# Performance work log

Hardware: AMD Instinct MI355X
Metric: run time of the kernel (lower is better)

## Reference

```python
import jax, jax.numpy as jnp
import numpy as np

SR = 16000
NFFT = 512
HOP = 160
D_MIC = 0.05
SPEED = 343.0
PRE = 0.97
ALPHA, BETA, GAMMA = 0.5, 0.3, 0.2
MAXLEN = 40000
N_ANGLES = 181
T = 6400000

# ---- constant buffers (match torch register_buffer setup) ----
_freqs = np.fft.rfftfreq(NFFT, 1.0 / SR).astype(np.float32)            # [F]
_angles = np.linspace(0.0, 180.0, N_ANGLES).astype(np.float32)         # [A]
_tau = -(D_MIC * np.cos(np.deg2rad(_angles))) / SPEED
_phase = (2.0 * np.pi) * _tau[:, None] * _freqs[None, :]               # [A, F]
STEER_R = jnp.asarray(np.cos(_phase).astype(np.float32))
STEER_I = jnp.asarray(np.sin(_phase).astype(np.float32))
ANGLE_GRID = jnp.asarray(_angles)

_wl = SPEED / (_freqs + 1e-6)
_sr_res = D_MIC / _wl
_spatial = 1.0 / (1.0 + np.exp(-4.0 * (_sr_res - 0.1)))
_fw = 1.0 - np.exp(-((_freqs - SR / 6.0) ** 2) / (2.0 * (SR / 4.0) ** 2))
_alias = np.where(_sr_res < 0.5, np.ones_like(_freqs), np.exp(-2.0 * (_sr_res - 0.5) ** 2))
_cw = (_spatial * _fw * _alias)[None, :]
FREQ_W = jnp.asarray((_cw / (_cw.sum() + 1e-6)).astype(np.float32))    # [1, F]

_w = np.exp(np.linspace(-2.0, 0.0, MAXLEN).astype(np.float32))
TEMPORAL = jnp.asarray((_w / _w.sum()).reshape(1, 1, -1))              # [1,1,MAXLEN]

_n = np.arange(NFFT)
WINDOW = jnp.asarray((0.5 - 0.5 * np.cos(2.0 * np.pi * _n / NFFT)).astype(np.float32))
N_FRAMES = (T - NFFT) // HOP + 1
FRAME_IDX = jnp.asarray((np.arange(N_FRAMES)[:, None] * HOP + _n[None, :]).astype(np.int32))


def _stft(x):
    # x: [1, 1, T] -> (real, imag) each [1, F, n_frames]
    frames = x[:, 0, :][:, FRAME_IDX] * WINDOW       # [1, n_frames, NFFT]
    spec = jnp.fft.rfft(frames, axis=-1)             # [1, n_frames, F]
    spec = jnp.swapaxes(spec, 1, 2)                  # [1, F, n_frames]
    return jnp.real(spec).astype(jnp.float32), jnp.imag(spec).astype(jnp.float32)


def _preproc(w):
    w = w * (1.0 / 32768.0)
    w = w - jnp.mean(w, axis=-1, keepdims=True)
    return jnp.concatenate([w[:, :, :1], w[:, :, 1:] - PRE * w[:, :, :-1]], axis=-1)


def _mvdr_scores(mic_wav_0, mic_wav_1):
    r0, i0 = _stft(_preproc(mic_wav_0))
    r1, i1 = _stft(_preproc(mic_wav_1))
    p0 = r0 * r0 + i0 * i0
    p1 = r1 * r1 + i1 * i1
    r01 = r0 * r1 + i0 * i1
    i01 = i0 * r1 - r0 * i1
    wts = TEMPORAL[..., : p0.shape[-1]]
    R00 = (p0 * wts).sum(2)                          # [1, F]
    R11 = (p1 * wts).sum(2)
    R01r = (r01 * wts).sum(2)
    R01i = (i01 * wts).sum(2)
    trace = (R00 + R11) * 0.5
    det = R00 * R11 - (R01r ** 2 + R01i ** 2) + 1e-6 * trace
    inv_det = 1.0 / det
    iR00 = R11 * inv_det
    iR11 = R00 * inv_det
    iR01r = -R01r * inv_det
    iR01i = -R01i * inv_det
    qf = iR01r * STEER_R + iR01i * STEER_I           # [A, F] (B=1 broadcast)
    qf = iR00 + iR11 + qf + qf
    mvdr = 1.0 / (qf + 1e-6)
    logp = jnp.log(mvdr + 1e-6)
    geometric = jnp.exp((logp * FREQ_W).sum(-1))     # [A]
    arithmetic = (mvdr * FREQ_W).sum(-1)
    peak_w = jax.nn.softmax(mvdr + mvdr, axis=-1)
    peak = (mvdr * peak_w * FREQ_W).sum(-1)
    return ALPHA * geometric + BETA * arithmetic + GAMMA * peak


def setup_inputs() -> dict:
    key = jax.random.key(0)
    k0, k1 = jax.random.split(key)
    mic_wav_0 = jax.random.normal(k0, (1, 1, T), jnp.float32) * 8000.0
    noise = jax.random.normal(k1, (1, 1, T), jnp.float32) * 8000.0
    # correlated second channel with a small time shift (plausible TDOA)
    mic_wav_1 = 0.7 * jnp.roll(mic_wav_0, 3, axis=-1) + 0.3 * noise
    return {"mic_wav_0": mic_wav_0, "mic_wav_1": mic_wav_1}


def reference(mic_wav_0, mic_wav_1):
    scores = _mvdr_scores(mic_wav_0, mic_wav_1)      # [A]
    return ANGLE_GRID[jnp.argmax(scores, axis=-1)]
```

## Files before the change

### kernel.cpp

```cpp
#include <hip/hip_runtime.h>
#include <math.h>

#ifndef M_PI
#define M_PI 3.14159265358979323846
#endif

#define HOP 160
#define NBLK_MAX 2048
#define PSLOTS 1036

__device__ __forceinline__ float wave_reduce(float v) {
    for (int off = 32; off > 0; off >>= 1) v += __shfl_down(v, off, 64);
    return v;
}

__device__ __forceinline__ void dft8(float* xr, float* xi) {
    const float s = 0.70710678118654752440f;
    float t0r = xr[0] + xr[4], t0i = xi[0] + xi[4];
    float t1r = xr[0] - xr[4], t1i = xi[0] - xi[4];
    float t2r = xr[2] + xr[6], t2i = xi[2] + xi[6];
    float t3r = xr[2] - xr[6], t3i = xi[2] - xi[6];
    float E0r = t0r + t2r, E0i = t0i + t2i;
    float E2r = t0r - t2r, E2i = t0i - t2i;
    float E1r = t1r + t3i, E1i = t1i - t3r;
    float E3r = t1r - t3i, E3i = t1i + t3r;
    float u0r = xr[1] + xr[5], u0i = xi[1] + xi[5];
    float u1r = xr[1] - xr[5], u1i = xi[1] - xi[5];
    float u2r = xr[3] + xr[7], u2i = xi[3] + xi[7];
    float u3r = xr[3] - xr[7], u3i = xi[3] - xi[7];
    float O0r = u0r + u2r, O0i = u0i + u2i;
    float O2r = u0r - u2r, O2i = u0i - u2i;
    float O1r = u1r + u3i, O1i = u1i - u3r;
    float O3r = u1r - u3i, O3i = u1i + u3r;
    float T1r = s * (O1r + O1i), T1i = s * (O1i - O1r);
    float T2r = O2i,             T2i = -O2r;
    float T3r = s * (O3i - O3r), T3i = -s * (O3r + O3i);
    xr[0] = E0r + O0r; xi[0] = E0i + O0i;
    xr[4] = E0r - O0r; xi[4] = E0i - O0i;
    xr[1] = E1r + T1r; xi[1] = E1i + T1i;
    xr[5] = E1r - T1r; xi[5] = E1i - T1i;
    xr[2] = E2r + T2r; xi[2] = E2i + T2i;
    xr[6] = E2r - T2r; xi[6] = E2i - T2i;
    xr[3] = E3r + T3r; xi[3] = E3i + T3i;
    xr[7] = E3r - T3r; xi[7] = E3i - T3i;
}

__device__ __forceinline__ void cmul_t(float& zr, float& zi, float tr, float ti) {
    float r = zr * tr - zi * ti;
    float i = zr * ti + zi * tr;
    zr = r; zi = i;
}

__global__ __launch_bounds__(256) void stft_fft_kernel(
        const float* __restrict__ x0, const float* __restrict__ x1,
        float* __restrict__ partials,
        int T, int nframes, int fpb, int nblocks, int cs,
        float invS, float kslope)
{
    __shared__ float smem[4608];
    const int tid = threadIdx.x;
    const int w = tid >> 6, l = tid & 63;
    float* buf = smem + w * 1152;
    const int n0 = l & 7, hi = l >> 3;
    const int pl = (64 - l) & 63;
    const int b1r = n0 + 72 * hi;
    const int b2w = hi + 72 * n0;

    float c0 = 0.f, c1 = 0.f;
    {
        int lo = blockIdx.x * cs;
        int hi2 = lo + cs; if (hi2 > T) hi2 = T;
        for (int i = lo + tid; i < hi2; i += 256) { c0 += x0[i]; c1 += x1[i]; }
        c0 = wave_reduce(c0); c1 = wave_reduce(c1);
        if (l == 0) { smem[2 * w] = c0; smem[2 * w + 1] = c1; }
    }
    __syncthreads();
    const float c0T = (smem[0] + smem[2]) + (smem[4] + smem[6]);
    const float c1T = (smem[1] + smem[3]) + (smem[5] + smem[7]);
    __syncthreads();

    float winv[8];
#pragma unroll
    for (int j = 0; j < 8; ++j)
        winv[j] = (0.5f - 0.5f * cosf((float)(2.0 * M_PI / 512.0) * (float)(l + 64 * j)))
                  * (1.0f / 32768.0f);
    float t1r[8], t1i[8], t2r[8], t2i[8];
#pragma unroll
    for (int j = 0; j < 8; ++j) {
        sincosf((float)(-2.0 * M_PI / 64.0) * (float)(j * hi), &t1i[j], &t1r[j]);
        sincosf((float)(-2.0 * M_PI / 512.0) * (float)(j * l), &t2i[j], &t2r[j]);
    }

    float A[8];
    float Wr[5], Wi[5];
    float L0r = 0.f, L0i = 0.f, L7r = 0.f, L7i = 0.f;
#pragma unroll
    for (int r = 0; r < 8; ++r) A[r] = 0.f;
#pragma unroll
    for (int r = 0; r < 5; ++r) { Wr[r] = 0.f; Wi[r] = 0.f; }

    int f0 = blockIdx.x * fpb;
    int f1 = f0 + fpb; if (f1 > nframes) f1 = nframes;

    for (int f = f0 + w; f < f1; f += 4) {
        int base = f * HOP;
        float wt = expf(fmaf(kslope, (float)f, -2.0f)) * invS;

        float zr[8], zi[8];
#pragma unroll
        for (int j = 0; j < 8; ++j) {
            int t = base + l + 64 * j;
            int tp = t - 1;
            if (j == 0) tp = (tp < 0) ? 0 : tp;
            float d0 = fmaf(-0.97f, x0[tp], x0[t]);
            float d1 = fmaf(-0.97f, x1[tp], x1[t]);
            zr[j] = d0 * winv[j];
            zi[j] = d1 * winv[j];
        }

        dft8(zr, zi);

#pragma unroll
        for (int k2 = 0; k2 < 8; ++k2) {
            buf[l + 72 * k2] = zr[k2];
            buf[l + 72 * k2 + 576] = zi[k2];
        }
#pragma unroll
        for (int j = 0; j < 8; ++j) {
            zr[j] = buf[b1r + 8 * j];
            zi[j] = buf[b1r + 8 * j + 576];
        }
#pragma unroll
        for (int j = 1; j < 8; ++j) cmul_t(zr[j], zi[j], t1r[j], t1i[j]);
        dft8(zr, zi);

#pragma unroll
        for (int k1 = 0; k1 < 8; ++k1) {
            buf[b2w + 8 * k1] = zr[k1];
            buf[b2w + 8 * k1 + 576] = zi[k1];
        }
#pragma unroll
        for (int j = 0; j < 8; ++j) {
            zr[j] = buf[l + 72 * j];
            zi[j] = buf[l + 72 * j + 576];
        }
#pragma unroll
        for (int j = 1; j < 8; ++j) cmul_t(zr[j], zi[j], t2r[j], t2i[j]);
        dft8(zr, zi);

#pragma unroll
        for (int r = 0; r < 8; ++r) {
            float u = fmaf(zr[r], zr[r], zi[r] * zi[r]);
            A[r] = fmaf(wt, u, A[r]);
        }
        L0r = fmaf(wt, zr[0], L0r); L0i = fmaf(wt, zi[0], L0i);
        L7r = fmaf(wt, zr[7], L7r); L7i = fmaf(wt, zi[7], L7i);

#pragma unroll
        for (int r = 0; r < 4; ++r) {
            float br = __shfl(zr[7 - r], pl, 64);
            float bi = __shfl(zi[7 - r], pl, 64);
            if (l == 0) { br = zr[(8 - r) & 7]; bi = zi[(8 - r) & 7]; }
            float wr = fmaf(zr[r], br, -(zi[r] * bi));
            float wi = fmaf(zr[r], bi, zi[r] * br);
            Wr[r] = fmaf(wt, wr, Wr[r]);
            Wi[r] = fmaf(wt, wi, Wi[r]);
        }
        {
            float wr = fmaf(zr[4], zr[4], -(zi[4] * zi[4]));
            float wi = 2.f * zr[4] * zi[4];
            Wr[4] = fmaf(wt, wr, Wr[4]);
            Wi[4] = fmaf(wt, wi, Wi[4]);
        }
    }

    float R00[4], R11[4], R01r[4], R01i[4];
#pragma unroll
    for (int r = 0; r < 4; ++r) {
        float ap = __shfl(A[7 - r], pl, 64);
        if (l == 0) ap = A[(8 - r) & 7];
        R00[r]  = 0.25f * (A[r] + ap + 2.f * Wr[r]);
        R11[r]  = 0.25f * (A[r] + ap - 2.f * Wr[r]);
        R01r[r] = 0.5f  * Wi[r];
        R01i[r] = 0.25f * (A[r] - ap);
    }

    __syncthreads();
    float (*red)[PSLOTS] = (float (*)[PSLOTS])smem;
#pragma unroll
    for (int r = 0; r < 4; ++r) {
        int k = l + 64 * r;
        red[w][0 * 257 + k] = R00[r];
        red[w][1 * 257 + k] = R11[r];
        red[w][2 * 257 + k] = R01r[r];
        red[w][3 * 257 + k] = R01i[r];
    }
    if (l == 0) {
        red[w][0 * 257 + 256] = 0.5f * (A[4] + Wr[4]);
        red[w][1 * 257 + 256] = 0.5f * (A[4] - Wr[4]);
        red[w][2 * 257 + 256] = 0.5f * Wi[4];
        red[w][3 * 257 + 256] = 0.f;
        red[w][1028] = L0r;
        red[w][1029] = L0i;
    }
    if (l == 1) {
        red[w][1030] = L0r;
        red[w][1031] = L0i;
    }
    if (l == 63) {
        red[w][1032] = L7r;
        red[w][1033] = L7i;
    }
    if (l == 2) { red[w][1034] = 0.f; red[w][1035] = 0.f; }
    __syncthreads();
    for (int s = tid; s < PSLOTS; s += 256) {
        float v = (red[0][s] + red[1][s]) + (red[2][s] + red[3][s]);
        if (s == 1034) v = c0T;
        if (s == 1035) v = c1T;
        partials[(size_t)blockIdx.x * PSLOTS + s] = v;
    }
}

__global__ __launch_bounds__(256) void reduce_kernel(
        const float* __restrict__ partials, float* __restrict__ R, int nblocks)
{
    int s = blockIdx.x;
    int tid = threadIdx.x, lane = tid & 63, w = tid >> 6;
    float v = 0.f;
    for (int i = tid; i < nblocks; i += 256) v += partials[(size_t)i * PSLOTS + s];
    __shared__ float red[4];
    v = wave_reduce(v);
    if (lane == 0) red[w] = v;
    __syncthreads();
    if (tid == 0) R[s] = (red[0] + red[1]) + (red[2] + red[3]);
}

__global__ __launch_bounds__(64) void score_kernel(
        const float* __restrict__ R, float* __restrict__ scores,
        float Sw, float invT32768)
{
    int a = blockIdx.x;
    int l = threadIdx.x;

    float rad = (float)a * (float)(M_PI / 180.0);
    float tau = -(0.05f * cosf(rad)) / 343.0f;
    float t2  = (float)(2.0 * M_PI) * tau;

    float dr = 0.03f * R[1034] * invT32768;
    float di = 0.03f * R[1035] * invT32768;
    float dd  = dr * dr + di * di;
    float d2r = dr * dr - di * di;
    float d2i = 2.f * dr * di;

    float fwsum = 0.f;
    float geo = 0.f, ari = 0.f;
    float m = -1e30f, se = 0.f, pe = 0.f;

    for (int q = 0; q < 5; ++q) {
        int kk = l + 64 * q;
        if (kk > 256) break;
        float R00  = R[0 * 257 + kk];
        float R11  = R[1 * 257 + kk];
        float R01r = R[2 * 257 + kk];
        float R01i = R[3 * 257 + kk];

        if (q == 0 && l == 0) {
            float Lr = R[1028], Li = R[1029];
            float dA  = -512.f * (dr * Lr + di * Li) + 65536.f * dd * Sw;
            float dLr = dr * Lr - di * Li;
            float dLi = dr * Li + di * Lr;
            float dWr = -512.f * dLr + 65536.f * Sw * d2r;
            float dWi = -512.f * dLi + 65536.f * Sw * d2i;
            R00  += 0.5f * (dA + dWr);
            R11  += 0.5f * (dA - dWr);
            R01r += 0.5f * dWi;
        }
        if (q == 0 && l == 1) {
            float L1r = R[1030], L1i = R[1031];
            float L5r = R[1032], L5i = R[1033];
            float dA1 = 256.f * (dr * L1r + di * L1i) + 16384.f * dd * Sw;
            float dA5 = 256.f * (dr * L5r + di * L5i) + 16384.f * dd * Sw;
            float Sr = L1r + L5r, Si = L1i + L5i;
            float dWr = 128.f * (dr * Sr - di * Si) + 16384.f * Sw * d2r;
            float dWi = 128.f * (dr * Si + di * Sr) + 16384.f * Sw * d2i;
            R00  += 0.25f * (dA1 + dA5 + 2.f * dWr);
            R11  += 0.25f * (dA1 + dA5 - 2.f * dWr);
            R01r += 0.5f  * dWi;
            R01i += 0.25f * (dA1 - dA5);
        }

        float trace = (R00 + R11) * 0.5f;
        float det = R00 * R11 - (R01r * R01r + R01i * R01i) + 1e-6f * trace;
        float inv_det = 1.0f / det;
        float Sd = (R11 + R00) * inv_det;
        float qr = -R01r * inv_det;
        float qi = -R01i * inv_det;

        float fq = 31.25f * (float)kk;
        float wl = 343.0f / (fq + 1e-6f);
        float sr = 0.05f / wl;
        float spatial = 1.0f / (1.0f + expf(-4.0f * (sr - 0.1f)));
        float dq = fq - (float)(16000.0 / 6.0);
        float fwq = 1.0f - expf(-(dq * dq) / (float)(2.0 * 4000.0 * 4000.0));
        float alias = (sr < 0.5f) ? 1.0f : expf(-2.0f * (sr - 0.5f) * (sr - 0.5f));
        float fw = spatial * fwq * alias;
        fwsum += fw;

        float cr, ci;
        sincosf(t2 * fq, &ci, &cr);
        float t  = qr * cr + qi * ci;
        float qf = Sd + t + t;
        float mv = 1.0f / (qf + 1e-6f);

        geo = fmaf(logf(mv + 1e-6f), fw, geo);
        ari = fmaf(mv, fw, ari);
        float x = mv + mv;
        if (x > m) {
            float sc = expf(m - x);
            se = fmaf(se, sc, 1.0f);
            pe = fmaf(pe, sc, mv * fw);
            m = x;
        } else {
            float e = expf(x - m);
            se += e;
            pe = fmaf(mv * fw, e, pe);
        }
    }

    for (int off = 1; off < 64; off <<= 1) {
        fwsum += __shfl_xor(fwsum, off, 64);
        geo   += __shfl_xor(geo, off, 64);
        ari   += __shfl_xor(ari, off, 64);
        float mo = __shfl_xor(m, off, 64);
        float so = __shfl_xor(se, off, 64);
        float po = __shfl_xor(pe, off, 64);
        float mm = fmaxf(m, mo);
        float e1 = expf(m - mm), e2 = expf(mo - mm);
        se = fmaf(se, e1, so * e2);
        pe = fmaf(pe, e1, po * e2);
        m = mm;
    }
    if (l == 0) {
        float invcw = 1.0f / (fwsum + 1e-6f);
        float geon = geo * invcw;
        float arin = ari * invcw;
        float peak = (pe * invcw) / se;
        scores[a] = 0.5f * expf(geon) + 0.3f * arin + 0.2f * peak;
    }
}

__global__ __launch_bounds__(256) void argmax_kernel(
        const float* __restrict__ scores, float* __restrict__ out)
{
    int tid = threadIdx.x, lane = tid & 63, w = tid >> 6;
    float v = (tid < 181) ? scores[tid] : -1e30f;
    int   i = tid;
    for (int off = 1; off < 64; off <<= 1) {
        float vo = __shfl_xor(v, off, 64);
        int   io = __shfl_xor(i, off, 64);
        if (vo > v || (vo == v && io < i)) { v = vo; i = io; }
    }
    __shared__ float rv[4];
    __shared__ int   ri[4];
    if (lane == 0) { rv[w] = v; ri[w] = i; }
    __syncthreads();
    if (tid == 0) {
        float bv = rv[0]; int bi = ri[0];
        for (int q = 1; q < 4; ++q) {
            if (rv[q] > bv || (rv[q] == bv && ri[q] < bi)) { bv = rv[q]; bi = ri[q]; }
        }
        out[0] = (float)bi;
    }
}

extern "C" void kernel_launch(void* const* d_in, const int* in_sizes, int n_in,
                              void* d_out, int out_size, void* d_ws, size_t ws_size,
                              hipStream_t stream) {
    const float* x0 = (const float*)d_in[0];
    const float* x1 = (const float*)d_in[1];
    float* out = (float*)d_out;
    int T = in_sizes[0];
    int nframes = (T - 512) / HOP + 1;

    double Stot = 0.0, Spart = 0.0;
    for (int j = 0; j < 40000; ++j) {
        double e = exp(-2.0 + 2.0 * (double)j / 39999.0);
        Stot += e;
        if (j < nframes) Spart += e;
    }
    float invS = (float)(1.0 / Stot);
    float kslope = (float)(2.0 / 39999.0);
    float Sw = (float)(Spart / Stot);
    float invT32768 = (float)(1.0 / ((double)T * 32768.0));

    float* ws = (float*)d_ws;
    float* Rbuf     = ws;
    float* scores   = ws + 2048;
    float* partials = ws + 4096;

    long availf = (long)(ws_size / 4) - 4096;
    int nblocks = (int)(availf / PSLOTS);
    if (nblocks > NBLK_MAX) nblocks = NBLK_MAX;
    if (nblocks < 1) nblocks = 1;
    int fpb = (nframes + nblocks - 1) / nblocks;
    int cs  = (T + nblocks - 1) / nblocks;

    stft_fft_kernel<<<nblocks, 256, 0, stream>>>(x0, x1, partials,
                                                 T, nframes, fpb, nblocks, cs,
                                                 invS, kslope);
    reduce_kernel<<<PSLOTS, 256, 0, stream>>>(partials, Rbuf, nblocks);
    score_kernel<<<181, 64, 0, stream>>>(Rbuf, scores, Sw, invT32768);
    argmax_kernel<<<1, 256, 0, stream>>>(scores, out);
}
```

Before: 70.04 us.

## Replace partials buffer and reduce kernel with atomic accumulation into R

The STFT kernel now atomically adds each block's per-slot sums into a zeroed global R buffer, removing the partials buffer and the separate reduce kernel launch. A small init kernel clears R first, and the grid is fixed at 4096 blocks instead of being sized from workspace. This saves a launch and the partials write/read traffic, but adds contention from 4096 blocks each making 1036 atomic adds to the same addresses. It also makes the float summation order nondeterministic.

```diff
diff --git a/kernel.cpp b/kernel.cpp
--- a/kernel.cpp
+++ b/kernel.cpp
@@ -6,7 +6,7 @@
 #endif
 
 #define HOP 160
-#define NBLK_MAX 2048
+#define NBLK 4096
 #define PSLOTS 1036
 
 __device__ __forceinline__ float wave_reduce(float v) {
@@ -51,10 +51,15 @@
     zr = r; zi = i;
 }
 
+__global__ __launch_bounds__(256) void init_kernel(float* __restrict__ R) {
+    int i = blockIdx.x * 256 + threadIdx.x;
+    if (i < PSLOTS) R[i] = 0.f;
+}
+
 __global__ __launch_bounds__(256) void stft_fft_kernel(
         const float* __restrict__ x0, const float* __restrict__ x1,
-        float* __restrict__ partials,
-        int T, int nframes, int fpb, int nblocks, int cs,
+        float* __restrict__ Rbuf,
+        int T, int nframes, int fpb, int cs,
         float invS, float kslope)
 {
     __shared__ float smem[4608];
@@ -217,22 +222,8 @@
         float v = (red[0][s] + red[1][s]) + (red[2][s] + red[3][s]);
         if (s == 1034) v = c0T;
         if (s == 1035) v = c1T;
-        partials[(size_t)blockIdx.x * PSLOTS + s] = v;
-    }
-}
-
-__global__ __launch_bounds__(256) void reduce_kernel(
-        const float* __restrict__ partials, float* __restrict__ R, int nblocks)
-{
-    int s = blockIdx.x;
-    int tid = threadIdx.x, lane = tid & 63, w = tid >> 6;
-    float v = 0.f;
-    for (int i = tid; i < nblocks; i += 256) v += partials[(size_t)i * PSLOTS + s];
-    __shared__ float red[4];
-    v = wave_reduce(v);
-    if (lane == 0) red[w] = v;
-    __syncthreads();
-    if (tid == 0) R[s] = (red[0] + red[1]) + (red[2] + red[3]);
+        atomicAdd(&Rbuf[s], v);
+    }
 }
 
 __global__ __launch_bounds__(64) void score_kernel(
@@ -394,21 +385,16 @@
     float invT32768 = (float)(1.0 / ((double)T * 32768.0));
 
     float* ws = (float*)d_ws;
-    float* Rbuf     = ws;
-    float* scores   = ws + 2048;
-    float* partials = ws + 4096;
-
-    long availf = (long)(ws_size / 4) - 4096;
-    int nblocks = (int)(availf / PSLOTS);
-    if (nblocks > NBLK_MAX) nblocks = NBLK_MAX;
-    if (nblocks < 1) nblocks = 1;
-    int fpb = (nframes + nblocks - 1) / nblocks;
-    int cs  = (T + nblocks - 1) / nblocks;
-
-    stft_fft_kernel<<<nblocks, 256, 0, stream>>>(x0, x1, partials,
-                                                 T, nframes, fpb, nblocks, cs,
-                                                 invS, kslope);
-    reduce_kernel<<<PSLOTS, 256, 0, stream>>>(partials, Rbuf, nblocks);
+    float* Rbuf   = ws;
+    float* scores = ws + 2048;
+
+    int fpb = (nframes + NBLK - 1) / NBLK;
+    int cs  = (T + NBLK - 1) / NBLK;
+
+    init_kernel<<<(PSLOTS + 255) / 256, 256, 0, stream>>>(Rbuf);
+    stft_fft_kernel<<<NBLK, 256, 0, stream>>>(x0, x1, Rbuf,
+                                              T, nframes, fpb, cs,
+                                              invS, kslope);
     score_kernel<<<181, 64, 0, stream>>>(Rbuf, scores, Sw, invT32768);
     argmax_kernel<<<1, 256, 0, stream>>>(scores, out);
 }
```

New measurement: 133.2 us. +90.2%, slower.

## Use 512-thread blocks, fewer blocks, and precomputed twiddle table

Applied to the files above, without the earlier changes.

Doubles the STFT block size to 8 waves and halves the grid to 1024 blocks, which halves the per-block partial output and the work of the cross-block reduction. The per-thread window and twiddle sincos/cos computation moves into a one-block setup kernel that writes a table the main kernel then loads. In exchange there is an extra kernel launch, more shared memory per block (which may lower occupancy), and the workspace-size check on block count is removed.

```diff
diff --git a/kernel.cpp b/kernel.cpp
--- a/kernel.cpp
+++ b/kernel.cpp
@@ -6,7 +6,8 @@
 #endif
 
 #define HOP 160
-#define NBLK_MAX 2048
+#define NBLK 1024
+#define BDIM 512
 #define PSLOTS 1036
 
 __device__ __forceinline__ float wave_reduce(float v) {
@@ -51,13 +52,27 @@
     zr = r; zi = i;
 }
 
-__global__ __launch_bounds__(256) void stft_fft_kernel(
+__global__ __launch_bounds__(512) void twsetup_kernel(float* __restrict__ tw) {
+    int tid = threadIdx.x;
+    int j = tid >> 6, l = tid & 63, hi = l >> 3;
+    tw[tid] = (0.5f - 0.5f * cosf((float)(2.0 * M_PI / 512.0) * (float)(l + 64 * j)))
+              * (1.0f / 32768.0f);
+    float s1, c1, s2, c2;
+    sincosf((float)(-2.0 * M_PI / 64.0) * (float)(j * hi), &s1, &c1);
+    sincosf((float)(-2.0 * M_PI / 512.0) * (float)(j * l), &s2, &c2);
+    tw[512 + tid]  = c1;
+    tw[1024 + tid] = s1;
+    tw[1536 + tid] = c2;
+    tw[2048 + tid] = s2;
+}
+
+__global__ __launch_bounds__(512) void stft_fft_kernel(
         const float* __restrict__ x0, const float* __restrict__ x1,
-        float* __restrict__ partials,
-        int T, int nframes, int fpb, int nblocks, int cs,
+        const float* __restrict__ tw, float* __restrict__ partials,
+        int T, int nframes, int fpb, int cs,
         float invS, float kslope)
 {
-    __shared__ float smem[4608];
+    __shared__ float smem[9216];
     const int tid = threadIdx.x;
     const int w = tid >> 6, l = tid & 63;
     float* buf = smem + w * 1152;
@@ -70,25 +85,24 @@
     {
         int lo = blockIdx.x * cs;
         int hi2 = lo + cs; if (hi2 > T) hi2 = T;
-        for (int i = lo + tid; i < hi2; i += 256) { c0 += x0[i]; c1 += x1[i]; }
+        for (int i = lo + tid; i < hi2; i += BDIM) { c0 += x0[i]; c1 += x1[i]; }
         c0 = wave_reduce(c0); c1 = wave_reduce(c1);
         if (l == 0) { smem[2 * w] = c0; smem[2 * w + 1] = c1; }
     }
     __syncthreads();
-    const float c0T = (smem[0] + smem[2]) + (smem[4] + smem[6]);
-    const float c1T = (smem[1] + smem[3]) + (smem[5] + smem[7]);
-    __syncthreads();
-
-    float winv[8];
-#pragma unroll
-    for (int j = 0; j < 8; ++j)
-        winv[j] = (0.5f - 0.5f * cosf((float)(2.0 * M_PI / 512.0) * (float)(l + 64 * j)))
-                  * (1.0f / 32768.0f);
-    float t1r[8], t1i[8], t2r[8], t2i[8];
+    float c0T = 0.f, c1T = 0.f;
+#pragma unroll
+    for (int q = 0; q < 8; ++q) { c0T += smem[2 * q]; c1T += smem[2 * q + 1]; }
+    __syncthreads();
+
+    float winv[8], t1r[8], t1i[8], t2r[8], t2i[8];
 #pragma unroll
     for (int j = 0; j < 8; ++j) {
-        sincosf((float)(-2.0 * M_PI / 64.0) * (float)(j * hi), &t1i[j], &t1r[j]);
-        sincosf((float)(-2.0 * M_PI / 512.0) * (float)(j * l), &t2i[j], &t2r[j]);
+        winv[j] = tw[j * 64 + l];
+        t1r[j]  = tw[512 + j * 64 + l];
+        t1i[j]  = tw[1024 + j * 64 + l];
+        t2r[j]  = tw[1536 + j * 64 + l];
+        t2i[j]  = tw[2048 + j * 64 + l];
     }
 
     float A[8];
@@ -102,7 +116,7 @@
     int f0 = blockIdx.x * fpb;
     int f1 = f0 + fpb; if (f1 > nframes) f1 = nframes;
 
-    for (int f = f0 + w; f < f1; f += 4) {
+    for (int f = f0 + w; f < f1; f += 8) {
         int base = f * HOP;
         float wt = expf(fmaf(kslope, (float)f, -2.0f)) * invS;
 
@@ -213,8 +227,10 @@
     }
     if (l == 2) { red[w][1034] = 0.f; red[w][1035] = 0.f; }
     __syncthreads();
-    for (int s = tid; s < PSLOTS; s += 256) {
-        float v = (red[0][s] + red[1][s]) + (red[2][s] + red[3][s]);
+    for (int s = tid; s < PSLOTS; s += BDIM) {
+        float v = 0.f;
+#pragma unroll
+        for (int q = 0; q < 8; ++q) v += red[q][s];
         if (s == 1034) v = c0T;
         if (s == 1035) v = c1T;
         partials[(size_t)blockIdx.x * PSLOTS + s] = v;
@@ -396,19 +412,17 @@
     float* ws = (float*)d_ws;
     float* Rbuf     = ws;
     float* scores   = ws + 2048;
-    float* partials = ws + 4096;
-
-    long availf = (long)(ws_size / 4) - 4096;
-    int nblocks = (int)(availf / PSLOTS);
-    if (nblocks > NBLK_MAX) nblocks = NBLK_MAX;
-    if (nblocks < 1) nblocks = 1;
-    int fpb = (nframes + nblocks - 1) / nblocks;
-    int cs  = (T + nblocks - 1) / nblocks;
-
-    stft_fft_kernel<<<nblocks, 256, 0, stream>>>(x0, x1, partials,
-                                                 T, nframes, fpb, nblocks, cs,
-                                                 invS, kslope);
-    reduce_kernel<<<PSLOTS, 256, 0, stream>>>(partials, Rbuf, nblocks);
+    float* tw       = ws + 3072;
+    float* partials = ws + 8192;
+
+    int fpb = (nframes + NBLK - 1) / NBLK;
+    int cs  = (T + NBLK - 1) / NBLK;
+
+    twsetup_kernel<<<1, 512, 0, stream>>>(tw);
+    stft_fft_kernel<<<NBLK, BDIM, 0, stream>>>(x0, x1, tw, partials,
+                                               T, nframes, fpb, cs,
+                                               invS, kslope);
+    reduce_kernel<<<PSLOTS, 256, 0, stream>>>(partials, Rbuf, NBLK);
     score_kernel<<<181, 64, 0, stream>>>(Rbuf, scores, Sw, invT32768);
     argmax_kernel<<<1, 256, 0, stream>>>(scores, out);
 }
```

After: 84.38 us. 20.5% more time.
